# Kernel tuning notes

Hardware: AMD Instinct MI355X
Metric: run time of the kernel (lower is better)

The kernel has to match this reference:

```python
import jax, jax.numpy as jnp
import numpy as np
import math

NUM_BUCKETS = 32
MAX_DISTANCE = 128


def _relative_position_buckets(seq_len):
    # bidirectional T5-style buckets, matching the torch reference exactly
    pos = jnp.arange(seq_len)
    rp = pos[None, :] - pos[:, None]                # [S, S]
    nb = NUM_BUCKETS // 2                            # bidirectional halving
    buckets = (rp > 0).astype(jnp.int32) * nb
    rp = jnp.abs(rp)
    max_exact = nb // 2
    is_small = rp < max_exact
    rp_f = jnp.maximum(rp, 1).astype(jnp.float32)    # avoid log(0); masked by is_small
    rp_large = max_exact + (
        jnp.log(rp_f / max_exact) / math.log(MAX_DISTANCE / max_exact) * (nb - max_exact)
    ).astype(jnp.int32)                              # trunc toward zero, like .to(torch.long)
    rp_large = jnp.minimum(rp_large, nb - 1)
    return buckets + jnp.where(is_small, rp, rp_large)  # [S, S] int32 in [0, 31]


def setup_inputs() -> dict:
    key = jax.random.key(0)
    kq, kk, kv, km, kb = jax.random.split(key, 5)
    B, H, S, D = 4, 4, 2048, 64
    return {
        "query": jax.random.normal(kq, (B, H, S, D), dtype=jnp.float32),
        "key": jax.random.normal(kk, (B, H, S, D), dtype=jnp.float32),
        "value": jax.random.normal(kv, (B, H, S, D), dtype=jnp.float32),
        "mask": jax.random.randint(km, (B, 1, 1, S), 0, 2, dtype=jnp.int32),
        "bias_table": jax.random.normal(kb, (512, 4), dtype=jnp.float32) * 0.02,
    }


def reference(query, key, value, mask, bias_table):
    B, H, S, D = query.shape
    attn = jnp.einsum("bhqd,bhkd->bhqk", query, key)          # [B,H,S,S]
    rel = _relative_position_buckets(S)                        # [S,S]
    bias = bias_table[rel]                                     # [S,S,H]
    bias = jnp.transpose(bias, (2, 0, 1))[None]                # [1,H,S,S]
    scores = (attn + bias) / math.sqrt(D)                      # bias added pre-scale, as in torch
    scores = jnp.where(mask == 0, jnp.float32(-1e9), scores)
    p_attn = jax.nn.softmax(scores, axis=-1)
    out = jnp.einsum("bhqk,bhkd->bhqd", p_attn, value)
    return out, p_attn
```

## Files before the change

kernel.cpp:

```cpp
#include <hip/hip_runtime.h>
#include <math.h>

typedef __attribute__((ext_vector_type(4))) float f32x4;
typedef _Float16 f16x8 __attribute__((ext_vector_type(8)));
typedef _Float16 f16x4v __attribute__((ext_vector_type(4)));

#define S_LEN 2048
#define D_HEAD 64
#define C2 0.18033688011112043f
#define PKSTRIDE 328

static __device__ __forceinline__ float exp2v(float x) {
    float r; asm("v_exp_f32 %0, %1" : "=v"(r) : "v"(x)); return r;
}

static __device__ __forceinline__ void gl_lds16(const void* g, void* l) {
    __builtin_amdgcn_global_load_lds(
        (const __attribute__((address_space(1))) unsigned int*)g,
        (__attribute__((address_space(3))) unsigned int*)l, 16, 0, 0);
}

__global__ void prep_bias(const float* __restrict__ table, float* __restrict__ bias_d) {
    int idx = blockIdx.x * blockDim.x + threadIdx.x;
    if (idx >= 4096) return;
    int delta = idx - 2047;
    int bpos = (delta > 0) ? 16 : 0;
    int ad = delta < 0 ? -delta : delta;
    int rel;
    if (ad < 8) {
        rel = bpos + ad;
    } else {
        float rp = (float)ad;
        int lg = 8 + (int)(logf(rp / 8.0f) / 2.772588722239781f * 8.0f);
        if (lg > 15) lg = 15;
        rel = bpos + lg;
    }
    #pragma unroll
    for (int h = 0; h < 4; ++h)
        bias_d[h * 4096 + idx] = C2 * table[rel * 4 + h];
}

__global__ void prep_half(const float* __restrict__ src, _Float16* __restrict__ dst) {
    size_t i8 = ((size_t)blockIdx.x * 256 + threadIdx.x) * 8;
    f32x4 a = *(const f32x4*)(src + i8);
    f32x4 b = *(const f32x4*)(src + i8 + 4);
    f16x8 h;
    h[0] = (_Float16)a[0]; h[1] = (_Float16)a[1];
    h[2] = (_Float16)a[2]; h[3] = (_Float16)a[3];
    h[4] = (_Float16)b[0]; h[5] = (_Float16)b[1];
    h[6] = (_Float16)b[2]; h[7] = (_Float16)b[3];
    *(f16x8*)(dst + i8) = h;
}

__global__ void prep_vt(const float* __restrict__ V, _Float16* __restrict__ vt) {
    __shared__ float tile[64][65];
    const int bh = blockIdx.y;
    const int k0 = blockIdx.x * 64;
    const int t = threadIdx.x;
    {
        int r = t >> 2, c0 = (t & 3) * 16;
        const float* src = V + ((size_t)bh * S_LEN + k0 + r) * D_HEAD + c0;
        #pragma unroll
        for (int i = 0; i < 16; i += 4) {
            f32x4 v = *(const f32x4*)(src + i);
            tile[r][c0 + i + 0] = v[0];
            tile[r][c0 + i + 1] = v[1];
            tile[r][c0 + i + 2] = v[2];
            tile[r][c0 + i + 3] = v[3];
        }
    }
    __syncthreads();
    {
        int d = t >> 2, kc = (t & 3) * 16;
        size_t ob = ((size_t)bh * D_HEAD + d) * S_LEN + k0 + kc;
        #pragma unroll
        for (int half = 0; half < 2; ++half) {
            f16x8 hv;
            #pragma unroll
            for (int i = 0; i < 8; ++i)
                hv[i] = (_Float16)tile[kc + half * 8 + i][d];
            *(f16x8*)(vt + ob + half * 8) = hv;
        }
    }
}

__launch_bounds__(512, 4)
__global__ void attn_main(const float* __restrict__ Q, const int* __restrict__ mask,
                          const float* __restrict__ bias2,
                          const _Float16* __restrict__ kh_g,
                          const _Float16* __restrict__ vt_g,
                          float* __restrict__ outp, float* __restrict__ p_out) {
    __shared__ __align__(16) char smem[75264];
    _Float16* pkbuf = (_Float16*)(smem + 32768);
    float* stats = (float*)(smem + 74752);

    const int tid = threadIdx.x;
    const int w = tid >> 6, l = tid & 63;
    const int wq = w & 3, wk = w >> 2;
    const int g = l >> 4, lq = l & 15;
    const int r7 = lq & 7;
    const int bid = blockIdx.x;
    const int bh = bid & 15, b = bh >> 2, h = bh & 3;
    const int q0 = (bid >> 4) * 64;

    const float* Qp = Q + (size_t)bh * (S_LEN * D_HEAD);
    const int* mp = mask + b * S_LEN;
    const _Float16* khp = kh_g + (size_t)bh * (S_LEN * D_HEAD);
    const _Float16* vhp = vt_g + (size_t)bh * (S_LEN * D_HEAD);

    _Float16* qarea = (_Float16*)smem;
    {
        int sr = tid >> 3, tb = tid & 7;
        const float* src = Qp + (size_t)(q0 + sr) * D_HEAD + tb * 8;
        f32x4 a = *(const f32x4*)src;
        f32x4 c = *(const f32x4*)(src + 4);
        f16x8 hv;
        hv[0] = (_Float16)a[0]; hv[1] = (_Float16)a[1];
        hv[2] = (_Float16)a[2]; hv[3] = (_Float16)a[3];
        hv[4] = (_Float16)c[0]; hv[5] = (_Float16)c[1];
        hv[6] = (_Float16)c[2]; hv[7] = (_Float16)c[3];
        *(f16x8*)(qarea + sr * 64 + ((tb ^ (sr & 7)) * 8)) = hv;
    }
    __syncthreads();
    f16x8 qf[2];
    const int qrow = 16 * wq + lq;
    #pragma unroll
    for (int c = 0; c < 2; ++c)
        qf[c] = *(const f16x8*)(qarea + qrow * 64 + ((4 * c + g) ^ r7) * 8);
    __syncthreads();

    const int qq = q0 + qrow;

    const int rr3 = tid >> 3;
    const int ub0 = (((tid & 7) ^ (rr3 & 7)) * 8);
    const _Float16* s1a = khp + (size_t)rr3 * 64 + ub0;
    gl_lds16(s1a, smem + tid * 16);
    gl_lds16(s1a + 4096, smem + 8192 + tid * 16);
    __syncthreads();

    const int* mP1 = mp + 64 * wk + 4 * g;
    const float* bP1 = bias2 + h * 4096 + 2047 - qq + 64 * wk + 4 * g;
    float lsum = 0.0f;
    for (int t = 0; t < 16; ++t) {
        const char* kb = smem + (t & 1) * 16384;
        int4 mv[4]; f32x4 bv[4];
        #pragma unroll
        for (int t2 = 0; t2 < 4; ++t2) {
            mv[t2] = *(const int4*)(mP1 + 16 * t2);
            bv[t2] = *(const f32x4*)(bP1 + 16 * t2);
        }
        if (t < 15) {
            s1a += 8192;
            char* nb = smem + ((t + 1) & 1) * 16384 + tid * 16;
            gl_lds16(s1a, nb);
            gl_lds16(s1a + 4096, nb + 8192);
        }
        __builtin_amdgcn_sched_barrier(0);
        #pragma unroll
        for (int t2 = 0; t2 < 4; ++t2) {
            const int krow = 64 * wk + 16 * t2 + lq;
            f32x4 acc = {0.f, 0.f, 0.f, 0.f};
            #pragma unroll
            for (int c = 0; c < 2; ++c) {
                f16x8 af = *(const f16x8*)(kb + krow * 128 + ((4 * c + g) ^ r7) * 16);
                acc = __builtin_amdgcn_mfma_f32_16x16x32_f16(af, qf[c], acc, 0, 0, 0);
            }
            float s0 = mv[t2].x ? fmaf(acc[0], C2, bv[t2][0]) : -1e9f;
            float s1 = mv[t2].y ? fmaf(acc[1], C2, bv[t2][1]) : -1e9f;
            float s2 = mv[t2].z ? fmaf(acc[2], C2, bv[t2][2]) : -1e9f;
            float s3 = mv[t2].w ? fmaf(acc[3], C2, bv[t2][3]) : -1e9f;
            lsum += exp2v(s0) + exp2v(s1) + exp2v(s2) + exp2v(s3);
        }
        mP1 += 128; bP1 += 128;
        asm volatile("s_waitcnt vmcnt(0)" ::: "memory");
        __builtin_amdgcn_sched_barrier(0);
        __builtin_amdgcn_s_barrier();
        __builtin_amdgcn_sched_barrier(0);
    }
    lsum += __shfl_xor(lsum, 16);
    lsum += __shfl_xor(lsum, 32);
    if (g == 0) stats[wk * 64 + qrow] = lsum;

    const _Float16* sKh = khp + (size_t)rr3 * 64 + ub0;
    const _Float16* sVh = vhp + (size_t)rr3 * 2048 + ub0;
    gl_lds16(sKh, smem + tid * 16);
    gl_lds16(sVh, smem + 8192 + tid * 16);
    __syncthreads();
    float lr2q;
    {
        float L = stats[qrow] + stats[64 + qrow];
        float lg; asm("v_log_f32 %0, %1" : "=v"(lg) : "v"(L));
        lr2q = -lg;
    }

    f32x4 acco[4] = {{0.f,0.f,0.f,0.f},{0.f,0.f,0.f,0.f},{0.f,0.f,0.f,0.f},{0.f,0.f,0.f,0.f}};
    const int* mP = mp + 32 * wk + 4 * g;
    const float* bP = bias2 + h * 4096 + 2047 - qq + 32 * wk + 4 * g;
    const int kAoff0 = (32 * wk + lq) * 128;
    const int voffb = lq * 128 + ((4 * wk + g) ^ r7) * 16;
    _Float16* pwrb = pkbuf + qrow * PKSTRIDE + 32 * wk + 4 * g;
    const _Float16* prdb = pkbuf + qrow * PKSTRIDE + 32 * wk + 8 * g;
    const _Float16* frb = pkbuf + (size_t)(8 * w) * PKSTRIDE + (l & 15) * 4;
    float* pFf = p_out + (size_t)bh * (S_LEN * S_LEN)
               + (size_t)(q0 + 8 * w) * S_LEN + (l >> 4) * 64 + (l & 15) * 4;
    int slot = 0;
    int s0 = 0;

    for (int t = 0; t < 32; ++t) {
        const int cb = (t & 1) * 16384;
        const bool fl = (t > 0) && ((t & 3) == 0);
        int4 mv[2]; f32x4 bv[2];
        #pragma unroll
        for (int t2 = 0; t2 < 2; ++t2) {
            mv[t2] = *(const int4*)(mP + 16 * t2);
            bv[t2] = *(const f32x4*)(bP + 16 * t2);
        }
        if (t < 31) {
            sKh += 4096; sVh += 64;
            char* d0 = smem + ((t + 1) & 1) * 16384 + tid * 16;
            gl_lds16(sKh, d0);
            gl_lds16(sVh, d0 + 8192);
        }
        if (fl) {
            int sl = s0 + (l >> 4); if (sl >= 5) sl -= 5;
            const _Float16* fr = frb + sl * 64;
            #pragma unroll
            for (int i = 0; i < 8; ++i) {
                f16x4v v = *(const f16x4v*)(fr + i * PKSTRIDE);
                f32x4 wv;
                wv[0] = (float)v[0]; wv[1] = (float)v[1];
                wv[2] = (float)v[2]; wv[3] = (float)v[3];
                *(f32x4*)(pFf + (size_t)i * S_LEN) = wv;
            }
            pFf += 256;
            s0 -= 1; if (s0 < 0) s0 += 5;
        }
        __builtin_amdgcn_sched_barrier(0);
        _Float16* pwr = pwrb + slot * 64;
        #pragma unroll
        for (int t2 = 0; t2 < 2; ++t2) {
            const char* kbase = smem + cb + kAoff0 + t2 * 2048;
            f32x4 acc = {0.f, 0.f, 0.f, 0.f};
            #pragma unroll
            for (int c = 0; c < 2; ++c) {
                f16x8 ah = *(const f16x8*)(kbase + ((4 * c + g) ^ r7) * 16);
                acc = __builtin_amdgcn_mfma_f32_16x16x32_f16(ah, qf[c], acc, 0, 0, 0);
            }
            float p0 = exp2v(mv[t2].x ? fmaf(acc[0], C2, bv[t2][0]) + lr2q : -1e9f);
            float p1 = exp2v(mv[t2].y ? fmaf(acc[1], C2, bv[t2][1]) + lr2q : -1e9f);
            float p2 = exp2v(mv[t2].z ? fmaf(acc[2], C2, bv[t2][2]) + lr2q : -1e9f);
            float p3 = exp2v(mv[t2].w ? fmaf(acc[3], C2, bv[t2][3]) + lr2q : -1e9f);
            f16x4v ph;
            ph[0] = (_Float16)p0; ph[1] = (_Float16)p1;
            ph[2] = (_Float16)p2; ph[3] = (_Float16)p3;
            *(f16x4v*)(pwr + 16 * t2) = ph;
        }
        const f16x8 pf = *(const f16x8*)(prdb + slot * 64);
        #pragma unroll
        for (int n = 0; n < 4; ++n) {
            const f16x8 bhf = *(const f16x8*)(smem + cb + 8192 + voffb + n * 2048);
            acco[n] = __builtin_amdgcn_mfma_f32_16x16x32_f16(pf, bhf, acco[n], 0, 0, 0);
        }
        mP += 64; bP += 64;
        slot = (slot == 4) ? 0 : slot + 1;
        if (fl) { asm volatile("s_waitcnt vmcnt(8)" ::: "memory"); }
        else    { asm volatile("s_waitcnt vmcnt(0)" ::: "memory"); }
        __builtin_amdgcn_sched_barrier(0);
        __builtin_amdgcn_s_barrier();
        __builtin_amdgcn_sched_barrier(0);
    }
    {
        int sl = s0 + (l >> 4); if (sl >= 5) sl -= 5;
        const _Float16* fr = frb + sl * 64;
        #pragma unroll
        for (int i = 0; i < 8; ++i) {
            f16x4v v = *(const f16x4v*)(fr + i * PKSTRIDE);
            f32x4 wv;
            wv[0] = (float)v[0]; wv[1] = (float)v[1];
            wv[2] = (float)v[2]; wv[3] = (float)v[3];
            *(f32x4*)(pFf + (size_t)i * S_LEN) = wv;
        }
    }

    float* ored = (float*)smem;
    __syncthreads();
    if (wk == 1) {
        #pragma unroll
        for (int n = 0; n < 4; ++n)
            #pragma unroll
            for (int r = 0; r < 4; ++r)
                ored[(wq * 16 + 4 * g + r) * 64 + 16 * n + lq] = acco[n][r];
    }
    __syncthreads();
    if (wk == 0) {
        #pragma unroll
        for (int n = 0; n < 4; ++n) {
            #pragma unroll
            for (int r = 0; r < 4; ++r) {
                float v = acco[n][r] + ored[(wq * 16 + 4 * g + r) * 64 + 16 * n + lq];
                outp[((size_t)bh * S_LEN + q0 + 16 * wq + 4 * g + r) * D_HEAD + 16 * n + lq] = v;
            }
        }
    }
}

extern "C" void kernel_launch(void* const* d_in, const int* in_sizes, int n_in,
                              void* d_out, int out_size, void* d_ws, size_t ws_size,
                              hipStream_t stream) {
    const float* Q = (const float*)d_in[0];
    const float* K = (const float*)d_in[1];
    const float* V = (const float*)d_in[2];
    const int* mask = (const int*)d_in[3];
    const float* table = (const float*)d_in[4];

    float* outp = (float*)d_out;
    float* p_out = outp + (size_t)4 * 4 * 2048 * 64;

    float* bias_d = (float*)d_ws;
    _Float16* kh = (_Float16*)((char*)d_ws + 65536);
    _Float16* vt = kh + (size_t)16 * S_LEN * D_HEAD;

    prep_bias<<<16, 256, 0, stream>>>(table, bias_d);
    prep_half<<<1024, 256, 0, stream>>>(K, kh);
    prep_vt<<<dim3(32, 16), 256, 0, stream>>>(V, vt);
    attn_main<<<512, 512, 0, stream>>>(Q, mask, bias_d, kh, vt, outp, p_out);
}
```

Baseline: 108.3 us.

## Replace 5-slot P ring buffer with per-wave double-buffered staging and flush every step

Replaces the 5-slot shared P buffer, which was flushed to global memory every fourth iteration, with a compact per-wave double buffer. The previous tile's probabilities are written out as fp32 on every iteration. This cuts LDS use from about 75 KB to about 54 KB, so launch bounds rise to 6 blocks per CU for more occupancy. The global P stores are now smaller and spread evenly across iterations, and the wait becomes a uniform vmcnt(2). The trade-off is a different store coalescing pattern and tighter register limits under the higher occupancy bound.

New measurement: 92.69 us (median of 2 runs). 14.4% less time.

```diff
diff --git a/kernel.cpp b/kernel.cpp
--- a/kernel.cpp
+++ b/kernel.cpp
@@ -8,7 +8,6 @@
 #define S_LEN 2048
 #define D_HEAD 64
 #define C2 0.18033688011112043f
-#define PKSTRIDE 328
 
 static __device__ __forceinline__ float exp2v(float x) {
     float r; asm("v_exp_f32 %0, %1" : "=v"(r) : "v"(x)); return r;
@@ -84,15 +83,15 @@
     }
 }
 
-__launch_bounds__(512, 4)
+__launch_bounds__(512, 6)
 __global__ void attn_main(const float* __restrict__ Q, const int* __restrict__ mask,
                           const float* __restrict__ bias2,
                           const _Float16* __restrict__ kh_g,
                           const _Float16* __restrict__ vt_g,
                           float* __restrict__ outp, float* __restrict__ p_out) {
-    __shared__ __align__(16) char smem[75264];
-    _Float16* pkbuf = (_Float16*)(smem + 32768);
-    float* stats = (float*)(smem + 74752);
+    __shared__ __align__(16) char smem[53760];
+    _Float16* pball = (_Float16*)(smem + 32768);
+    float* stats = (float*)(smem + 53248);
 
     const int tid = threadIdx.x;
     const int w = tid >> 6, l = tid & 63;
@@ -198,17 +197,16 @@
     const float* bP = bias2 + h * 4096 + 2047 - qq + 32 * wk + 4 * g;
     const int kAoff0 = (32 * wk + lq) * 128;
     const int voffb = lq * 128 + ((4 * wk + g) ^ r7) * 16;
-    _Float16* pwrb = pkbuf + qrow * PKSTRIDE + 32 * wk + 4 * g;
-    const _Float16* prdb = pkbuf + qrow * PKSTRIDE + 32 * wk + 8 * g;
-    const _Float16* frb = pkbuf + (size_t)(8 * w) * PKSTRIDE + (l & 15) * 4;
-    float* pFf = p_out + (size_t)bh * (S_LEN * S_LEN)
-               + (size_t)(q0 + 8 * w) * S_LEN + (l >> 4) * 64 + (l & 15) * 4;
-    int slot = 0;
-    int s0 = 0;
+    _Float16* pwr = pball + w * 1280 + lq * 40 + g * 4;
+    const _Float16* prd = pball + w * 1280 + lq * 40 + g * 8;
+    const _Float16* flb = pball + ((((l >> 3) & 1) * 4 + wq) * 1280)
+                        + (8 * wk + (l >> 4)) * 40 + (l & 7) * 4;
+    float* pF = p_out + (size_t)bh * (S_LEN * S_LEN)
+              + (size_t)(q0 + 16 * wq + 8 * wk + (l >> 4)) * S_LEN + (l & 15) * 4;
 
     for (int t = 0; t < 32; ++t) {
         const int cb = (t & 1) * 16384;
-        const bool fl = (t > 0) && ((t & 3) == 0);
+        const int cs = (t & 1) * 640;
         int4 mv[2]; f32x4 bv[2];
         #pragma unroll
         for (int t2 = 0; t2 < 2; ++t2) {
@@ -221,22 +219,19 @@
             gl_lds16(sKh, d0);
             gl_lds16(sVh, d0 + 8192);
         }
-        if (fl) {
-            int sl = s0 + (l >> 4); if (sl >= 5) sl -= 5;
-            const _Float16* fr = frb + sl * 64;
-            #pragma unroll
-            for (int i = 0; i < 8; ++i) {
-                f16x4v v = *(const f16x4v*)(fr + i * PKSTRIDE);
+        if (t > 0) {
+            const int ps = cs ^ 640;
+            #pragma unroll
+            for (int i = 0; i < 2; ++i) {
+                f16x4v v = *(const f16x4v*)(flb + ps + i * 160);
                 f32x4 wv;
                 wv[0] = (float)v[0]; wv[1] = (float)v[1];
                 wv[2] = (float)v[2]; wv[3] = (float)v[3];
-                *(f32x4*)(pFf + (size_t)i * S_LEN) = wv;
+                *(f32x4*)(pF + (size_t)(4 * i) * S_LEN) = wv;
             }
-            pFf += 256;
-            s0 -= 1; if (s0 < 0) s0 += 5;
-        }
-        __builtin_amdgcn_sched_barrier(0);
-        _Float16* pwr = pwrb + slot * 64;
+            pF += 64;
+        }
+        __builtin_amdgcn_sched_barrier(0);
         #pragma unroll
         for (int t2 = 0; t2 < 2; ++t2) {
             const char* kbase = smem + cb + kAoff0 + t2 * 2048;
@@ -253,32 +248,28 @@
             f16x4v ph;
             ph[0] = (_Float16)p0; ph[1] = (_Float16)p1;
             ph[2] = (_Float16)p2; ph[3] = (_Float16)p3;
-            *(f16x4v*)(pwr + 16 * t2) = ph;
-        }
-        const f16x8 pf = *(const f16x8*)(prdb + slot * 64);
+            *(f16x4v*)(pwr + cs + 16 * t2) = ph;
+        }
+        const f16x8 pf = *(const f16x8*)(prd + cs);
         #pragma unroll
         for (int n = 0; n < 4; ++n) {
             const f16x8 bhf = *(const f16x8*)(smem + cb + 8192 + voffb + n * 2048);
             acco[n] = __builtin_amdgcn_mfma_f32_16x16x32_f16(pf, bhf, acco[n], 0, 0, 0);
         }
         mP += 64; bP += 64;
-        slot = (slot == 4) ? 0 : slot + 1;
-        if (fl) { asm volatile("s_waitcnt vmcnt(8)" ::: "memory"); }
-        else    { asm volatile("s_waitcnt vmcnt(0)" ::: "memory"); }
+        asm volatile("s_waitcnt vmcnt(2) lgkmcnt(0)" ::: "memory");
         __builtin_amdgcn_sched_barrier(0);
         __builtin_amdgcn_s_barrier();
         __builtin_amdgcn_sched_barrier(0);
     }
     {
-        int sl = s0 + (l >> 4); if (sl >= 5) sl -= 5;
-        const _Float16* fr = frb + sl * 64;
-        #pragma unroll
-        for (int i = 0; i < 8; ++i) {
-            f16x4v v = *(const f16x4v*)(fr + i * PKSTRIDE);
+        #pragma unroll
+        for (int i = 0; i < 2; ++i) {
+            f16x4v v = *(const f16x4v*)(flb + 640 + i * 160);
             f32x4 wv;
             wv[0] = (float)v[0]; wv[1] = (float)v[1];
             wv[2] = (float)v[2]; wv[3] = (float)v[3];
-            *(f32x4*)(pFf + (size_t)i * S_LEN) = wv;
+            *(f32x4*)(pF + (size_t)(4 * i) * S_LEN) = wv;
         }
     }
 
```
